# Kernel optimization log

Measured on AMD Instinct MI355X. Metric: run time of the kernel, lower is better.

## Reference

```python
import jax, jax.numpy as jnp
import numpy as np

NUM_HEADS = 16
NUM_KV_HEADS = 4
HEAD_SIZE = 128
SCALE = 1.0 / np.sqrt(128.0).astype(np.float32)
NEG_INF = -1e30


def setup_inputs() -> dict:
    key = jax.random.key(0)
    kq, kk, kv = jax.random.split(key, 3)
    B, S = 2, 2048
    query = jax.random.normal(kq, (B, NUM_HEADS, S, HEAD_SIZE), dtype=jnp.float32)
    k = jax.random.normal(kk, (B, NUM_KV_HEADS, S, HEAD_SIZE), dtype=jnp.float32)
    v = jax.random.normal(kv, (B, NUM_KV_HEADS, S, HEAD_SIZE), dtype=jnp.float32)
    return {"query": query, "key": k, "value": v}


def _attn(query, key, value):
    # query: [B, H, S, D]; key/value: [B, Hkv, S, D]; GQA with group = H // Hkv
    B, H, S, D = query.shape
    Hkv = key.shape[1]
    G = H // Hkv
    q = query.reshape(B, Hkv, G, S, D)
    # scores: [B, Hkv, G, Sq, Sk]
    scores = jnp.einsum('bkgsd,bktd->bkgst', q, key) * jnp.float32(SCALE)
    causal = jnp.tril(jnp.ones((S, S), dtype=bool))  # [Sq, Sk]
    scores = jnp.where(causal, scores, jnp.float32(NEG_INF))
    probs = jax.nn.softmax(scores, axis=-1)
    out = jnp.einsum('bkgst,bktd->bkgsd', probs, value)  # [B, Hkv, G, S, D]
    out = out.reshape(B, H, S, D)
    # transpose(1,2).reshape -> [B, S, H*D]
    return out.transpose(0, 2, 1, 3).reshape(B, S, H * D)


def reference(query, key, value):
    return _attn(query, key, value)
```

## Files before the change

kernel.cpp:

```cpp
#include <hip/hip_runtime.h>


#define S_LEN 2048
#define DH    128
#define NH    16
#define NKVH  4
#define NB    2
#define TQ    128
#define TK    64
#define NQT   (S_LEN / TQ)
#define PROW  72
#define QSCALE 0.12752749610559243f

typedef __attribute__((ext_vector_type(8))) short short8;
typedef __attribute__((ext_vector_type(4))) float f32x4;

#if __has_builtin(__builtin_amdgcn_exp2f)
#define EX2(x) __builtin_amdgcn_exp2f(x)
#else
#define EX2(x) exp2f(x)
#endif

__device__ __forceinline__ unsigned short bf1(float a) {
    union { float f; unsigned u; } x; x.f = a;
    return (unsigned short)((x.u + 0x8000u) >> 16);
}
__device__ __forceinline__ unsigned pk2(float a, float b) {
    union { float f; unsigned u; } x, y; x.f = a; y.f = b;
    return ((x.u + 0x8000u) >> 16) | ((y.u + 0x8000u) & 0xffff0000u);
}
__device__ __forceinline__ void cp16(const void* g, void* lds) {
    __builtin_amdgcn_global_load_lds(
        (const __attribute__((address_space(1))) void*)g,
        (__attribute__((address_space(3))) void*)lds, 16, 0, 0);
}

__global__ __launch_bounds__(256, 4)
void prepack(const float* __restrict__ K, const float* __restrict__ V,
             unsigned short* __restrict__ Kb, unsigned short* __restrict__ Vt) {
    if (blockIdx.y == 0) {
        const long long flat = (long long)blockIdx.x * 2048 + threadIdx.x * 8;
        const int s = (int)(flat >> 7) & (S_LEN - 1);
        const int d0 = (int)flat & 127;
        const float* p = K + flat;
        float4 x = *(const float4*)p;
        float4 y = *(const float4*)(p + 4);
        const int cs = (d0 >> 3) ^ (s & 7);
        uint4 o;
        o.x = pk2(x.x, x.y); o.y = pk2(x.z, x.w);
        o.z = pk2(y.x, y.y); o.w = pk2(y.z, y.w);
        *(uint4*)(Kb + (flat & ~127LL) + cs * 8) = o;
    } else {
        const int x = blockIdx.x;
        const int bkvh = x >> 7, sblk = (x >> 2) & 31, q = x & 3;
        const int tid = threadIdx.x;
        __shared__ unsigned Lt[64][17];
        const float* base = V + (size_t)bkvh * S_LEN * DH + (size_t)sblk * 64 * DH + q * 32;
#pragma unroll
        for (int j = 0; j < 2; ++j) {
            const int e = tid + j * 256;
            const int s = e >> 3, c4 = e & 7;
            float4 v = *(const float4*)(base + (size_t)s * DH + c4 * 4);
            Lt[s][c4 * 2]     = pk2(v.x, v.y);
            Lt[s][c4 * 2 + 1] = pk2(v.z, v.w);
        }
        __syncthreads();
        const unsigned short* lt = (const unsigned short*)&Lt[0][0];
        const int d_loc = tid >> 3, pc = tid & 7;
        const int d = q * 32 + d_loc;
        const int c_log = pc ^ (d & 7);
        unsigned short vv[8];
#pragma unroll
        for (int j = 0; j < 8; ++j) {
            const int kp = c_log * 8 + j;
            const int kv = (kp & 3) * 16 + (kp >> 2);
            vv[j] = lt[kv * 34 + d_loc];
        }
        uint4 o;
        o.x = (unsigned)vv[0] | ((unsigned)vv[1] << 16);
        o.y = (unsigned)vv[2] | ((unsigned)vv[3] << 16);
        o.z = (unsigned)vv[4] | ((unsigned)vv[5] << 16);
        o.w = (unsigned)vv[6] | ((unsigned)vv[7] << 16);
        *(uint4*)(Vt + (size_t)bkvh * S_LEN * DH + (size_t)d * S_LEN + sblk * 64 + pc * 8) = o;
    }
}

__global__ __launch_bounds__(256, 2)
void attn_fwd(const float* __restrict__ Q,
              const unsigned short* __restrict__ Kb,
              const unsigned short* __restrict__ Vtg,
              float* __restrict__ O) {
    const int n  = blockIdx.x;
    const int x  = n & 15;
    const int h  = (n >> 4) & 15;
    const int b  = n >> 8;
    const int qt = b ? x : (NQT - 1 - x);
    const int kvh = h >> 2;

    const int tid  = threadIdx.x;
    const int w    = tid >> 6;
    const int lane = tid & 63;
    const int quad = lane >> 4;
    const int l16  = lane & 15;
    const int swz  = l16 & 7;

    __shared__ alignas(16) unsigned short Kl[TK][DH];
    __shared__ alignas(16) unsigned short Vl[DH][TK];
    __shared__ alignas(16) unsigned short Pl[TQ][PROW];

    const unsigned short* kb = Kb  + ((size_t)b * NKVH + kvh) * (size_t)(S_LEN * DH);
    const unsigned short* vb = Vtg + ((size_t)b * NKVH + kvh) * (size_t)(S_LEN * DH);

    const int wq0 = qt * TQ + w * 32;
    short8 aq[2][4];
#pragma unroll
    for (int sub = 0; sub < 2; ++sub) {
        const float* qp = Q + (((size_t)b * NH + h) * S_LEN + wq0 + sub * 16 + l16) * DH;
#pragma unroll
        for (int dc = 0; dc < 4; ++dc) {
            float4 xx = *(const float4*)(qp + dc * 32 + quad * 8);
            float4 yy = *(const float4*)(qp + dc * 32 + quad * 8 + 4);
            union { unsigned u[4]; short8 s; } t;
            t.u[0] = pk2(xx.x * QSCALE, xx.y * QSCALE);
            t.u[1] = pk2(xx.z * QSCALE, xx.w * QSCALE);
            t.u[2] = pk2(yy.x * QSCALE, yy.y * QSCALE);
            t.u[3] = pk2(yy.z * QSCALE, yy.w * QSCALE);
            aq[sub][dc] = t.s;
        }
    }

    f32x4 o[2][8];
#pragma unroll
    for (int sub = 0; sub < 2; ++sub)
#pragma unroll
        for (int ch = 0; ch < 8; ++ch) o[sub][ch] = (f32x4){0.f, 0.f, 0.f, 0.f};
    float lsum[2][4];
#pragma unroll
    for (int sub = 0; sub < 2; ++sub)
#pragma unroll
        for (int r = 0; r < 4; ++r) lsum[sub][r] = 0.f;

    const int nt  = 2 * qt + 2;
    const int ntw = 2 * qt + 1 + (w >> 1);

    for (int t = 0; t < nt; ++t) {
        const int j0 = t * TK;
        __syncthreads();
        {
            const char* ks = (const char*)(kb + (size_t)j0 * DH);
#pragma unroll
            for (int i = 0; i < 4; ++i)
                cp16(ks + w * 4096 + i * 1024 + lane * 16,
                     (char*)&Kl[0][0] + w * 4096 + i * 1024);
            const char* vs = (const char*)vb;
#pragma unroll
            for (int i = 0; i < 4; ++i) {
                const int row  = w * 32 + i * 8 + (lane >> 3);
                const int colB = (lane & 7) * 16;
                cp16(vs + (size_t)row * (S_LEN * 2) + j0 * 2 + colB,
                     (char*)&Vl[0][0] + w * 4096 + i * 1024);
            }
        }
        __syncthreads();

        if (t < ntw) {
            const bool diag = (t == ntw - 1);
            f32x4 s[2][4];
#pragma unroll
            for (int sub = 0; sub < 2; ++sub)
#pragma unroll
                for (int k4 = 0; k4 < 4; ++k4) s[sub][k4] = (f32x4){0.f, 0.f, 0.f, 0.f};
#pragma unroll
            for (int dc = 0; dc < 4; ++dc) {
#pragma unroll
                for (int k4 = 0; k4 < 4; ++k4) {
                    short8 bk = *(const short8*)&Kl[k4 * 16 + l16][((dc * 4 + quad) ^ swz) * 8];
                    s[0][k4] = __builtin_amdgcn_mfma_f32_16x16x32_bf16(aq[0][dc], bk, s[0][k4], 0, 0, 0);
                    s[1][k4] = __builtin_amdgcn_mfma_f32_16x16x32_bf16(aq[1][dc], bk, s[1][k4], 0, 0, 0);
                }
            }
#pragma unroll
            for (int sub = 0; sub < 2; ++sub) {
                const int rb = wq0 + sub * 16 + quad * 4;
#pragma unroll
                for (int r = 0; r < 4; ++r) {
                    float v0 = s[sub][0][r], v1 = s[sub][1][r];
                    float v2 = s[sub][2][r], v3 = s[sub][3][r];
                    if (diag) {
                        const int row = rb + r;
                        if (j0 + l16      > row) v0 = -1e30f;
                        if (j0 + 16 + l16 > row) v1 = -1e30f;
                        if (j0 + 32 + l16 > row) v2 = -1e30f;
                        if (j0 + 48 + l16 > row) v3 = -1e30f;
                    }
                    float p0 = EX2(v0), p1 = EX2(v1), p2 = EX2(v2), p3 = EX2(v3);
                    lsum[sub][r] += (p0 + p1) + (p2 + p3);
                    const int prow = w * 32 + sub * 16 + quad * 4 + r;
                    *(uint2*)&Pl[prow][l16 * 4] = make_uint2(pk2(p0, p1), pk2(p2, p3));
                }
            }
#pragma unroll
            for (int kc = 0; kc < 2; ++kc) {
                short8 ap0 = *(const short8*)&Pl[w * 32 + l16][kc * 32 + quad * 8];
                short8 ap1 = *(const short8*)&Pl[w * 32 + 16 + l16][kc * 32 + quad * 8];
#pragma unroll
                for (int ch = 0; ch < 8; ++ch) {
                    short8 bv = *(const short8*)&Vl[ch * 16 + l16][((kc * 4 + quad) ^ swz) * 8];
                    o[0][ch] = __builtin_amdgcn_mfma_f32_16x16x32_bf16(ap0, bv, o[0][ch], 0, 0, 0);
                    o[1][ch] = __builtin_amdgcn_mfma_f32_16x16x32_bf16(ap1, bv, o[1][ch], 0, 0, 0);
                }
            }
        }
    }

#pragma unroll
    for (int sub = 0; sub < 2; ++sub) {
#pragma unroll
        for (int r = 0; r < 4; ++r) {
            float rs = lsum[sub][r];
            rs += __shfl_xor(rs, 1);
            rs += __shfl_xor(rs, 2);
            rs += __shfl_xor(rs, 4);
            rs += __shfl_xor(rs, 8);
            const float invl = 1.f / rs;
            const int row = wq0 + sub * 16 + quad * 4 + r;
            float* op = O + ((size_t)b * S_LEN + row) * (NH * DH) + h * DH;
#pragma unroll
            for (int ch = 0; ch < 8; ++ch)
                op[ch * 16 + l16] = o[sub][ch][r] * invl;
        }
    }
}

extern "C" void kernel_launch(void* const* d_in, const int* in_sizes, int n_in,
                              void* d_out, int out_size, void* d_ws, size_t ws_size,
                              hipStream_t stream) {
    const float* Q = (const float*)d_in[0];
    const float* K = (const float*)d_in[1];
    const float* V = (const float*)d_in[2];
    float* O = (float*)d_out;
    unsigned short* Kb = (unsigned short*)d_ws;
    unsigned short* Vt = Kb + (size_t)NB * NKVH * S_LEN * DH;
    dim3 pgrid(NB * NKVH * (S_LEN / 16), 2);
    prepack<<<pgrid, 256, 0, stream>>>(K, V, Kb, Vt);
    attn_fwd<<<dim3(512), 256, 0, stream>>>(Q, Kb, Vt, O);
}
```

Before: 154.7 us.

## Double-buffer K/V tiles, swizzle P in LDS, and remap blocks by KV head

K and V tiles are now double-buffered in LDS: the next tile's async global-to-LDS copy is issued before the current tile's MFMAs, so the main loop needs one barrier per iteration instead of two and load latency can overlap compute. The padded P buffer is replaced by an XOR-swizzled 64-column layout to keep LDS bank conflicts down while saving space. Block indexing now groups blocks that share a KV head next to each other, which may improve L2 reuse of K/V. LDS use grows to about 80KB per block, which could reduce occupancy below the two blocks per CU the launch bounds request.

```diff
diff --git a/kernel.cpp b/kernel.cpp
--- a/kernel.cpp
+++ b/kernel.cpp
@@ -9,7 +9,6 @@
 #define TQ    128
 #define TK    64
 #define NQT   (S_LEN / TQ)
-#define PROW  72
 #define QSCALE 0.12752749610559243f
 
 typedef __attribute__((ext_vector_type(8))) short short8;
@@ -21,10 +20,6 @@
 #define EX2(x) exp2f(x)
 #endif
 
-__device__ __forceinline__ unsigned short bf1(float a) {
-    union { float f; unsigned u; } x; x.f = a;
-    return (unsigned short)((x.u + 0x8000u) >> 16);
-}
 __device__ __forceinline__ unsigned pk2(float a, float b) {
     union { float f; unsigned u; } x, y; x.f = a; y.f = b;
     return ((x.u + 0x8000u) >> 16) | ((y.u + 0x8000u) & 0xffff0000u);
@@ -90,12 +85,14 @@
               const unsigned short* __restrict__ Kb,
               const unsigned short* __restrict__ Vtg,
               float* __restrict__ O) {
-    const int n  = blockIdx.x;
-    const int x  = n & 15;
-    const int h  = (n >> 4) & 15;
-    const int b  = n >> 8;
-    const int qt = b ? x : (NQT - 1 - x);
-    const int kvh = h >> 2;
+    const int n   = blockIdx.x;
+    const int g   = n & 7;
+    const int b   = g >> 2;
+    const int kvh = g & 3;
+    const int kk  = n >> 3;
+    const int h   = kvh * 4 + (kk & 3);
+    const int x   = kk >> 2;
+    const int qt  = (x & 8) ? (x & 7) : (15 - (x & 7));
 
     const int tid  = threadIdx.x;
     const int w    = tid >> 6;
@@ -104,12 +101,32 @@
     const int l16  = lane & 15;
     const int swz  = l16 & 7;
 
-    __shared__ alignas(16) unsigned short Kl[TK][DH];
-    __shared__ alignas(16) unsigned short Vl[DH][TK];
-    __shared__ alignas(16) unsigned short Pl[TQ][PROW];
+    __shared__ alignas(16) unsigned short Kl[2][TK][DH];
+    __shared__ alignas(16) unsigned short Vl[2][DH][TK];
+    __shared__ alignas(16) unsigned short Pl[TQ][64];
 
     const unsigned short* kb = Kb  + ((size_t)b * NKVH + kvh) * (size_t)(S_LEN * DH);
     const unsigned short* vb = Vtg + ((size_t)b * NKVH + kvh) * (size_t)(S_LEN * DH);
+
+    const int nt  = 2 * qt + 2;
+    const int ntw = 2 * qt + 1 + (w >> 1);
+
+    auto stage = [&](int nb, int tt) {
+        const char* ks = (const char*)(kb + (size_t)tt * TK * DH);
+        char* kd = (char*)&Kl[nb][0][0] + w * 4096;
+#pragma unroll
+        for (int i = 0; i < 4; ++i)
+            cp16(ks + w * 4096 + i * 1024 + lane * 16, kd + i * 1024);
+        const char* vs = (const char*)vb + (size_t)tt * (TK * 2);
+        char* vd = (char*)&Vl[nb][0][0] + w * 4096;
+#pragma unroll
+        for (int i = 0; i < 4; ++i) {
+            const int row = w * 32 + i * 8 + (lane >> 3);
+            cp16(vs + (size_t)row * (S_LEN * 2) + (lane & 7) * 16, vd + i * 1024);
+        }
+    };
+
+    stage(0, 0);
 
     const int wq0 = qt * TQ + w * 32;
     short8 aq[2][4];
@@ -120,12 +137,12 @@
         for (int dc = 0; dc < 4; ++dc) {
             float4 xx = *(const float4*)(qp + dc * 32 + quad * 8);
             float4 yy = *(const float4*)(qp + dc * 32 + quad * 8 + 4);
-            union { unsigned u[4]; short8 s; } t;
-            t.u[0] = pk2(xx.x * QSCALE, xx.y * QSCALE);
-            t.u[1] = pk2(xx.z * QSCALE, xx.w * QSCALE);
-            t.u[2] = pk2(yy.x * QSCALE, yy.y * QSCALE);
-            t.u[3] = pk2(yy.z * QSCALE, yy.w * QSCALE);
-            aq[sub][dc] = t.s;
+            union { unsigned u[4]; short8 s; } tq;
+            tq.u[0] = pk2(xx.x * QSCALE, xx.y * QSCALE);
+            tq.u[1] = pk2(xx.z * QSCALE, xx.w * QSCALE);
+            tq.u[2] = pk2(yy.x * QSCALE, yy.y * QSCALE);
+            tq.u[3] = pk2(yy.z * QSCALE, yy.w * QSCALE);
+            aq[sub][dc] = tq.s;
         }
     }
 
@@ -140,30 +157,13 @@
 #pragma unroll
         for (int r = 0; r < 4; ++r) lsum[sub][r] = 0.f;
 
-    const int nt  = 2 * qt + 2;
-    const int ntw = 2 * qt + 1 + (w >> 1);
-
+    __syncthreads();
+
+    int cur = 0;
     for (int t = 0; t < nt; ++t) {
-        const int j0 = t * TK;
-        __syncthreads();
-        {
-            const char* ks = (const char*)(kb + (size_t)j0 * DH);
-#pragma unroll
-            for (int i = 0; i < 4; ++i)
-                cp16(ks + w * 4096 + i * 1024 + lane * 16,
-                     (char*)&Kl[0][0] + w * 4096 + i * 1024);
-            const char* vs = (const char*)vb;
-#pragma unroll
-            for (int i = 0; i < 4; ++i) {
-                const int row  = w * 32 + i * 8 + (lane >> 3);
-                const int colB = (lane & 7) * 16;
-                cp16(vs + (size_t)row * (S_LEN * 2) + j0 * 2 + colB,
-                     (char*)&Vl[0][0] + w * 4096 + i * 1024);
-            }
-        }
-        __syncthreads();
-
+        if (t + 1 < nt) stage(cur ^ 1, t + 1);
         if (t < ntw) {
+            const int j0 = t * TK;
             const bool diag = (t == ntw - 1);
             f32x4 s[2][4];
 #pragma unroll
@@ -174,7 +174,7 @@
             for (int dc = 0; dc < 4; ++dc) {
 #pragma unroll
                 for (int k4 = 0; k4 < 4; ++k4) {
-                    short8 bk = *(const short8*)&Kl[k4 * 16 + l16][((dc * 4 + quad) ^ swz) * 8];
+                    short8 bk = *(const short8*)&Kl[cur][k4 * 16 + l16][((dc * 4 + quad) ^ swz) * 8];
                     s[0][k4] = __builtin_amdgcn_mfma_f32_16x16x32_bf16(aq[0][dc], bk, s[0][k4], 0, 0, 0);
                     s[1][k4] = __builtin_amdgcn_mfma_f32_16x16x32_bf16(aq[1][dc], bk, s[1][k4], 0, 0, 0);
                 }
@@ -196,21 +196,27 @@
                     float p0 = EX2(v0), p1 = EX2(v1), p2 = EX2(v2), p3 = EX2(v3);
                     lsum[sub][r] += (p0 + p1) + (p2 + p3);
                     const int prow = w * 32 + sub * 16 + quad * 4 + r;
-                    *(uint2*)&Pl[prow][l16 * 4] = make_uint2(pk2(p0, p1), pk2(p2, p3));
+                    const int wcol = (l16 * 8) ^ ((prow & 7) << 4);
+                    *(uint2*)((char*)&Pl[0][0] + prow * 128 + wcol) =
+                        make_uint2(pk2(p0, p1), pk2(p2, p3));
                 }
             }
+            const int rx = (l16 & 7) << 4;
 #pragma unroll
             for (int kc = 0; kc < 2; ++kc) {
-                short8 ap0 = *(const short8*)&Pl[w * 32 + l16][kc * 32 + quad * 8];
-                short8 ap1 = *(const short8*)&Pl[w * 32 + 16 + l16][kc * 32 + quad * 8];
+                const int cb = kc * 64 + quad * 16;
+                short8 ap0 = *(const short8*)((const char*)&Pl[0][0] + (w * 32 + l16) * 128 + (cb ^ rx));
+                short8 ap1 = *(const short8*)((const char*)&Pl[0][0] + (w * 32 + 16 + l16) * 128 + (cb ^ rx));
 #pragma unroll
                 for (int ch = 0; ch < 8; ++ch) {
-                    short8 bv = *(const short8*)&Vl[ch * 16 + l16][((kc * 4 + quad) ^ swz) * 8];
+                    short8 bv = *(const short8*)&Vl[cur][ch * 16 + l16][((kc * 4 + quad) ^ swz) * 8];
                     o[0][ch] = __builtin_amdgcn_mfma_f32_16x16x32_bf16(ap0, bv, o[0][ch], 0, 0, 0);
                     o[1][ch] = __builtin_amdgcn_mfma_f32_16x16x32_bf16(ap1, bv, o[1][ch], 0, 0, 0);
                 }
             }
         }
+        __syncthreads();
+        cur ^= 1;
     }
 
 #pragma unroll
```

Measured after the change: 158.1 us. 1.02x slower.
